# Kernel tuning notes

Measured on AMD Instinct MI355X. Metric: run time of the kernel, lower is better.

## Reference

```python
import jax, jax.numpy as jnp
import numpy as np

N_HEAD = 8
D_Q = 1024
D_K = 1024  # d_k_original
DK = D_K // N_HEAD  # per-head dim = 128
B = 64
L = 2048


def setup_inputs() -> dict:
    key = jax.random.key(0)
    ks = jax.random.split(key, 8)
    std_q = np.sqrt(2.0 / (D_Q + DK)).astype(np.float32)
    std_k = np.sqrt(2.0 / (D_K + DK)).astype(np.float32)
    return {
        "q": jax.random.normal(ks[0], (B, D_Q), jnp.float32),
        "k": jax.random.normal(ks[1], (B, L, D_K), jnp.float32),
        "mask": jnp.zeros((B, L), jnp.bool_),
        # Linear weights stored torch-style: (out_features, in_features)
        "w_qs_w": jax.random.normal(ks[2], (N_HEAD * DK, D_Q), jnp.float32) * std_q,
        "w_qs_b": jnp.zeros((N_HEAD * DK,), jnp.float32),
        "w_ks_w": jax.random.normal(ks[3], (N_HEAD * DK, D_K), jnp.float32) * std_k,
        "w_ks_b": jnp.zeros((N_HEAD * DK,), jnp.float32),
        "w_vs_w": jax.random.normal(ks[4], (N_HEAD * DK, D_K), jnp.float32) * std_k,
        "w_vs_b": jnp.zeros((N_HEAD * DK,), jnp.float32),
    }


def reference(q, k, mask, w_qs_w, w_qs_b, w_ks_w, w_ks_b, w_vs_w, w_vs_b):
    # Dropouts are identity (eval mode).
    b, l, _ = k.shape
    temperature = jnp.sqrt(jnp.asarray(DK, q.dtype))
    # Projections: torch Linear y = x @ W.T + b
    qs = (q @ w_qs_w.T + w_qs_b).reshape(b, N_HEAD, DK)          # (b, n, dk)
    ks = (k @ w_ks_w.T + w_ks_b).reshape(b, l, N_HEAD, DK)       # (b, l, n, dk)
    vs = (k @ w_vs_w.T + w_vs_b).reshape(b, l, N_HEAD, DK)       # (b, l, n, dv)
    # Single-query per head attention scores: (b, n, l)
    attn = jnp.einsum("bnd,blnd->bnl", qs, ks) / temperature
    attn = jnp.where(mask[:, None, :], -jnp.inf, attn)
    attn = jax.nn.softmax(attn, axis=-1)
    # Weighted sum over l: (b, n, dv) -> (b, n*dv)
    output = jnp.einsum("bnl,blnd->bnd", attn, vs).reshape(b, N_HEAD * DK)
    # attn returned head-major like original: (n*b, l)
    attn_out = attn.transpose(1, 0, 2).reshape(N_HEAD * b, l)
    return (output, attn_out)
```

## Files before the change

kernel.cpp:

```cpp
#include <hip/hip_runtime.h>
#include <hip/hip_bf16.h>
#include <math.h>

#define B 64
#define L 2048
#define C 1024
#define NH 8
#define DK 128
#define SCALE 0.08838834764831845f

template<int CTRL, int RMASK = 0xF>
__device__ __forceinline__ float dppmov(float x) {
    return __int_as_float(__builtin_amdgcn_update_dpp(
        0, __float_as_int(x), CTRL, RMASK, 0xF, true));
}
__device__ __forceinline__ float wave_sum_dpp(float s) {
    s += dppmov<0x111>(s);
    s += dppmov<0x112>(s);
    s += dppmov<0x114>(s);
    s += dppmov<0x118>(s);
    s += dppmov<0x142, 0xa>(s);
    s += dppmov<0x143, 0xc>(s);
    return s;
}

__global__ void k_qs(const float* __restrict__ q, const float* __restrict__ wq,
                     const float* __restrict__ bq, float* __restrict__ qs) {
    int t = threadIdx.x, w = t >> 6, lane = t & 63;
    int j = blockIdx.x * 4 + w;
    float4 W[4];
#pragma unroll
    for (int kk = 0; kk < 4; kk++)
        W[kk] = *(const float4*)&wq[(size_t)j * C + kk * 256 + lane * 4];
    float bj = bq[j];
    for (int b = 0; b < B; b++) {
        float s = 0.f;
#pragma unroll
        for (int kk = 0; kk < 4; kk++) {
            float4 qv = *(const float4*)&q[(size_t)b * C + kk * 256 + lane * 4];
            s += W[kk].x * qv.x + W[kk].y * qv.y + W[kk].z * qv.z + W[kk].w * qv.w;
        }
        s = wave_sum_dpp(s);
        if (lane == 63) qs[(size_t)b * C + j] = s + bj;
    }
}

__global__ void k_qtilde(const float* __restrict__ qs, const float* __restrict__ wk,
                         float* __restrict__ qtilde) {
    int n = blockIdx.x >> 2, cc = blockIdx.x & 3, bg = blockIdx.y;
    int t = threadIdx.x;
    int c = cc * 256 + t;
    __shared__ float qss[8][128];
    for (int p = 0; p < 4; p++) {
        int e = p * 256 + t;
        int i = e >> 7, d = e & 127;
        qss[i][d] = qs[(size_t)(bg * 8 + i) * C + n * DK + d];
    }
    __syncthreads();
    float acc[8];
#pragma unroll
    for (int i = 0; i < 8; i++) acc[i] = 0.f;
    for (int d = 0; d < DK; d += 4) {
        float wv0 = wk[(size_t)(n * DK + d + 0) * C + c];
        float wv1 = wk[(size_t)(n * DK + d + 1) * C + c];
        float wv2 = wk[(size_t)(n * DK + d + 2) * C + c];
        float wv3 = wk[(size_t)(n * DK + d + 3) * C + c];
#pragma unroll
        for (int i = 0; i < 8; i++) {
            acc[i] += qss[i][d + 0] * wv0 + qss[i][d + 1] * wv1
                    + qss[i][d + 2] * wv2 + qss[i][d + 3] * wv3;
        }
    }
#pragma unroll
    for (int i = 0; i < 8; i++)
        qtilde[((size_t)(bg * 8 + i) * NH + n) * C + c] = acc[i] * SCALE;
}

__global__ __launch_bounds__(512, 2) void k_fused9(
    const float* __restrict__ kmat, const float* __restrict__ qtilde,
    const unsigned char* __restrict__ mask,
    float* __restrict__ pout,
    float* __restrict__ accpart,
    float* __restrict__ zpart) {
    const int b = blockIdx.x, lp = blockIdx.y;
    const int t = threadIdx.x, w = t >> 6, lane = t & 63;
    const int chunk = w >> 1;
    const int hg = w & 1;
    const int l0 = lp * 512 + chunk * 128;
    const int hl = lane & 3;

    __shared__ float ctxl[NH * C];
    __shared__ float zl[NH];

    float4 qt[4][4];
#pragma unroll
    for (int j = 0; j < 4; j++)
#pragma unroll
        for (int kk = 0; kk < 4; kk++)
            qt[j][kk] = *(const float4*)&qtilde[((size_t)b * NH + hg * 4 + j) * C + kk * 256 + lane * 4];

    float4 acc[4][4];
#pragma unroll
    for (int j = 0; j < 4; j++)
#pragma unroll
        for (int kk = 0; kk < 4; kk++) acc[j][kk] = make_float4(0.f, 0.f, 0.f, 0.f);
    float zacc = 0.f;

    const float* kp = kmat + ((size_t)b * L + l0) * C + lane * 4;
    const unsigned char* mp = mask + (size_t)b * L + l0;

    float4 kv[2][4];
#pragma unroll
    for (int kk = 0; kk < 4; kk++) kv[0][kk] = *(const float4*)(kp + kk * 256);

    for (int rb = 0; rb < 32; rb++) {
        uchar4 mb = *(const uchar4*)&mp[rb * 4];
        float ss[4];
#pragma unroll
        for (int rr = 0; rr < 4; rr++) {
            const int r = rb * 4 + rr;
            const int cur = r & 1;
            if (r < 127) {
                const float* np = kp + (size_t)(r + 1) * C;
#pragma unroll
                for (int kk = 0; kk < 4; kk++)
                    kv[cur ^ 1][kk] = *(const float4*)(np + kk * 256);
            }
            float s0 = 0.f, s1 = 0.f, s2 = 0.f, s3 = 0.f;
#pragma unroll
            for (int kk = 0; kk < 4; kk++) {
                float4 kq = kv[cur][kk];
                s0 += qt[0][kk].x * kq.x + qt[0][kk].y * kq.y + qt[0][kk].z * kq.z + qt[0][kk].w * kq.w;
                s1 += qt[1][kk].x * kq.x + qt[1][kk].y * kq.y + qt[1][kk].z * kq.z + qt[1][kk].w * kq.w;
                s2 += qt[2][kk].x * kq.x + qt[2][kk].y * kq.y + qt[2][kk].z * kq.z + qt[2][kk].w * kq.w;
                s3 += qt[3][kk].x * kq.x + qt[3][kk].y * kq.y + qt[3][kk].z * kq.z + qt[3][kk].w * kq.w;
            }
            float a01 = (lane & 1) ? s1 : s0;
            float g01 = (lane & 1) ? s0 : s1;
            float a23 = (lane & 1) ? s3 : s2;
            float g23 = (lane & 1) ? s2 : s3;
            float u  = a01 + dppmov<0xB1>(g01);
            float v2 = a23 + dppmov<0xB1>(g23);
            float keep = (lane & 2) ? v2 : u;
            float give = (lane & 2) ? u : v2;
            float v = keep + dppmov<0x4E>(give);
            v += dppmov<0x124>(v);
            v += dppmov<0x128>(v);
            v += __int_as_float(__builtin_amdgcn_ds_swizzle(
                     __float_as_int(v), 0x401F));
            v += __shfl_xor(v, 32, 64);
            unsigned char mk = (rr == 0) ? mb.x : (rr == 1) ? mb.y : (rr == 2) ? mb.z : mb.w;
            float p = __expf(mk ? -INFINITY : v);
            zacc += p;
            ss[rr] = p;
            float p1 = dppmov<0xB1>(p);
            float p2 = dppmov<0x4E>(p);
            float p3 = dppmov<0x4E>(p1);
#pragma unroll
            for (int kk = 0; kk < 4; kk++) {
                float4 kq = kv[cur][kk];
                acc[0][kk].x += p  * kq.x; acc[0][kk].y += p  * kq.y; acc[0][kk].z += p  * kq.z; acc[0][kk].w += p  * kq.w;
                acc[1][kk].x += p1 * kq.x; acc[1][kk].y += p1 * kq.y; acc[1][kk].z += p1 * kq.z; acc[1][kk].w += p1 * kq.w;
                acc[2][kk].x += p2 * kq.x; acc[2][kk].y += p2 * kq.y; acc[2][kk].z += p2 * kq.z; acc[2][kk].w += p2 * kq.w;
                acc[3][kk].x += p3 * kq.x; acc[3][kk].y += p3 * kq.y; acc[3][kk].z += p3 * kq.z; acc[3][kk].w += p3 * kq.w;
            }
        }
        if (lane < 4) {
            float4 o = make_float4(ss[0], ss[1], ss[2], ss[3]);
            *(float4*)&pout[((size_t)(hg * 4 + lane) * B + b) * L + l0 + rb * 4] = o;
        }
        __syncthreads();
    }

    for (int ph = 0; ph < 4; ph++) {
        if (chunk == ph) {
#pragma unroll
            for (int j = 0; j < 4; j++) {
                int h = hg * 4 + (hl ^ j);
                float* dst = &ctxl[(size_t)h * C + lane * 4];
                if (ph == 0) {
#pragma unroll
                    for (int kk = 0; kk < 4; kk++)
                        *(float4*)&dst[kk * 256] = acc[j][kk];
                } else {
#pragma unroll
                    for (int kk = 0; kk < 4; kk++) {
                        float4 o = *(const float4*)&dst[kk * 256];
                        float4 a = acc[j][kk];
                        o.x += a.x; o.y += a.y; o.z += a.z; o.w += a.w;
                        *(float4*)&dst[kk * 256] = o;
                    }
                }
            }
            if (lane < 4) {
                if (ph == 0) zl[hg * 4 + lane] = zacc;
                else         zl[hg * 4 + lane] += zacc;
            }
        }
        __syncthreads();
    }
    float* ap = accpart + ((size_t)b * 4 + lp) * (NH * C);
#pragma unroll
    for (int i = 0; i < 4; i++) {
        int idx = t * 16 + i * 4;
        *(float4*)&ap[idx] = *(const float4*)&ctxl[idx];
    }
    if (t < NH) zpart[((size_t)b * 4 + lp) * NH + t] = zl[t];
}

__global__ void k_combine2(const float* __restrict__ accpart, const float* __restrict__ zpart,
                           float* __restrict__ ctx, float* __restrict__ pout) {
    int b = blockIdx.x, cq = blockIdx.y;
    int t = threadIdx.x;
    int c = cq * 256 + t;
    __shared__ float zi[NH];
    if (t < NH) {
        float z = 0.f;
#pragma unroll
        for (int lpp = 0; lpp < 4; lpp++) z += zpart[((size_t)b * 4 + lpp) * NH + t];
        zi[t] = 1.0f / z;
    }
    __syncthreads();
#pragma unroll
    for (int n = 0; n < NH; n++) {
        float s = 0.f;
#pragma unroll
        for (int lpp = 0; lpp < 4; lpp++)
            s += accpart[(((size_t)b * 4 + lpp) * NH + n) * C + c];
        ctx[((size_t)b * NH + n) * C + c] = s * zi[n];
    }
#pragma unroll
    for (int n = 0; n < NH; n++) {
        float zin = zi[n];
        float2* pp = (float2*)&pout[((size_t)n * B + b) * L + cq * 512];
        float2 v = pp[t];
        v.x *= zin; v.y *= zin;
        pp[t] = v;
    }
}

__global__ void k_out(const float* __restrict__ ctx, const float* __restrict__ wv,
                      const float* __restrict__ bv, float* __restrict__ out) {
    int t = threadIdx.x, w = t >> 6, lane = t & 63;
    int j = blockIdx.x * 4 + w;
    int n = j >> 7;
    float4 W[4];
#pragma unroll
    for (int kk = 0; kk < 4; kk++)
        W[kk] = *(const float4*)&wv[(size_t)j * C + kk * 256 + lane * 4];
    float bj = bv[j];
    for (int b = 0; b < B; b++) {
        float s = 0.f;
#pragma unroll
        for (int kk = 0; kk < 4; kk++) {
            float4 cv = *(const float4*)&ctx[((size_t)b * NH + n) * C + kk * 256 + lane * 4];
            s += W[kk].x * cv.x + W[kk].y * cv.y + W[kk].z * cv.z + W[kk].w * cv.w;
        }
        s = wave_sum_dpp(s);
        if (lane == 63) out[(size_t)b * (NH * DK) + j] = s + bj;
    }
}

extern "C" void kernel_launch(void* const* d_in, const int* in_sizes, int n_in,
                              void* d_out, int out_size, void* d_ws, size_t ws_size,
                              hipStream_t stream) {
    const float* q    = (const float*)d_in[0];
    const float* kmat = (const float*)d_in[1];
    const unsigned char* mask = (const unsigned char*)d_in[2];
    const float* wq = (const float*)d_in[3];
    const float* bq = (const float*)d_in[4];
    const float* wk = (const float*)d_in[5];
    const float* wv = (const float*)d_in[7];
    const float* bv = (const float*)d_in[8];

    float* out  = (float*)d_out;
    float* attn = out + B * NH * DK;

    float* ws      = (float*)d_ws;
    float* qs      = ws;
    float* zpart   = ws;
    float* qtilde  = ws + 65536;
    float* ctx     = qtilde;
    float* accpart = ws + 65536 + 524288;

    hipLaunchKernelGGL(k_qs, dim3(256), dim3(256), 0, stream, q, wq, bq, qs);
    hipLaunchKernelGGL(k_qtilde, dim3(32, 8), dim3(256), 0, stream, qs, wk, qtilde);
    hipLaunchKernelGGL(k_fused9, dim3(64, 4), dim3(512), 0, stream,
                       kmat, qtilde, mask, attn, accpart, zpart);
    hipLaunchKernelGGL(k_combine2, dim3(64, 4), dim3(256), 0, stream,
                       accpart, zpart, ctx, attn);
    hipLaunchKernelGGL(k_out, dim3(256), dim3(256), 0, stream, ctx, wv, bv, out);
}
```

Baseline: 228.0 us.

## Deepen K row prefetch to two-row pairs and drop per-block barrier

The main fused kernel now keeps four K rows in registers as two ping-pong pairs, prefetching the next two rows while the current two are processed, instead of a single-row lookahead. It also removes the __syncthreads executed every 4-row block inside the streaming loop, leaving one barrier before the shared-memory reduction. This aims to put more memory loads in flight and stop waves from stalling each other. The extra 32 VGPRs of K buffering may raise register pressure under the 512x2 launch bound and risk spills.

```diff
diff --git a/kernel.cpp b/kernel.cpp
--- a/kernel.cpp
+++ b/kernel.cpp
@@ -76,7 +76,7 @@
         qtilde[((size_t)(bg * 8 + i) * NH + n) * C + c] = acc[i] * SCALE;
 }
 
-__global__ __launch_bounds__(512, 2) void k_fused9(
+__global__ __launch_bounds__(512, 2) void k_fused10(
     const float* __restrict__ kmat, const float* __restrict__ qtilde,
     const unsigned char* __restrict__ mask,
     float* __restrict__ pout,
@@ -109,69 +109,85 @@
     const float* kp = kmat + ((size_t)b * L + l0) * C + lane * 4;
     const unsigned char* mp = mask + (size_t)b * L + l0;
 
-    float4 kv[2][4];
-#pragma unroll
-    for (int kk = 0; kk < 4; kk++) kv[0][kk] = *(const float4*)(kp + kk * 256);
+    auto ROW = [&](const float4 (&kq4)[4], unsigned char mk, float& ssl) {
+        float s0 = 0.f, s1 = 0.f, s2 = 0.f, s3 = 0.f;
+#pragma unroll
+        for (int kk = 0; kk < 4; kk++) {
+            float4 kq = kq4[kk];
+            s0 += qt[0][kk].x * kq.x + qt[0][kk].y * kq.y + qt[0][kk].z * kq.z + qt[0][kk].w * kq.w;
+            s1 += qt[1][kk].x * kq.x + qt[1][kk].y * kq.y + qt[1][kk].z * kq.z + qt[1][kk].w * kq.w;
+            s2 += qt[2][kk].x * kq.x + qt[2][kk].y * kq.y + qt[2][kk].z * kq.z + qt[2][kk].w * kq.w;
+            s3 += qt[3][kk].x * kq.x + qt[3][kk].y * kq.y + qt[3][kk].z * kq.z + qt[3][kk].w * kq.w;
+        }
+        float a01 = (lane & 1) ? s1 : s0;
+        float g01 = (lane & 1) ? s0 : s1;
+        float a23 = (lane & 1) ? s3 : s2;
+        float g23 = (lane & 1) ? s2 : s3;
+        float u  = a01 + dppmov<0xB1>(g01);
+        float v2 = a23 + dppmov<0xB1>(g23);
+        float keep = (lane & 2) ? v2 : u;
+        float give = (lane & 2) ? u : v2;
+        float v = keep + dppmov<0x4E>(give);
+        v += dppmov<0x124>(v);
+        v += dppmov<0x128>(v);
+        v += __int_as_float(__builtin_amdgcn_ds_swizzle(
+                 __float_as_int(v), 0x401F));
+        v += __shfl_xor(v, 32, 64);
+        float p = __expf(mk ? -INFINITY : v);
+        zacc += p;
+        ssl = p;
+        float p1 = dppmov<0xB1>(p);
+        float p2 = dppmov<0x4E>(p);
+        float p3 = dppmov<0x4E>(p1);
+#pragma unroll
+        for (int kk = 0; kk < 4; kk++) {
+            float4 kq = kq4[kk];
+            acc[0][kk].x += p  * kq.x; acc[0][kk].y += p  * kq.y; acc[0][kk].z += p  * kq.z; acc[0][kk].w += p  * kq.w;
+            acc[1][kk].x += p1 * kq.x; acc[1][kk].y += p1 * kq.y; acc[1][kk].z += p1 * kq.z; acc[1][kk].w += p1 * kq.w;
+            acc[2][kk].x += p2 * kq.x; acc[2][kk].y += p2 * kq.y; acc[2][kk].z += p2 * kq.z; acc[2][kk].w += p2 * kq.w;
+            acc[3][kk].x += p3 * kq.x; acc[3][kk].y += p3 * kq.y; acc[3][kk].z += p3 * kq.z; acc[3][kk].w += p3 * kq.w;
+        }
+    };
+
+    float4 kA[2][4], kB[2][4];
+#pragma unroll
+    for (int kk = 0; kk < 4; kk++) {
+        kA[0][kk] = *(const float4*)(kp + 0 * C + kk * 256);
+        kA[1][kk] = *(const float4*)(kp + 1 * C + kk * 256);
+        kB[0][kk] = *(const float4*)(kp + 2 * C + kk * 256);
+        kB[1][kk] = *(const float4*)(kp + 3 * C + kk * 256);
+    }
 
     for (int rb = 0; rb < 32; rb++) {
         uchar4 mb = *(const uchar4*)&mp[rb * 4];
         float ss[4];
-#pragma unroll
-        for (int rr = 0; rr < 4; rr++) {
-            const int r = rb * 4 + rr;
-            const int cur = r & 1;
-            if (r < 127) {
-                const float* np = kp + (size_t)(r + 1) * C;
-#pragma unroll
-                for (int kk = 0; kk < 4; kk++)
-                    kv[cur ^ 1][kk] = *(const float4*)(np + kk * 256);
+        ROW(kA[0], mb.x, ss[0]);
+        ROW(kA[1], mb.y, ss[1]);
+        if (rb < 31) {
+            const float* np = kp + (size_t)(rb * 4 + 4) * C;
+#pragma unroll
+            for (int kk = 0; kk < 4; kk++) {
+                kA[0][kk] = *(const float4*)(np + kk * 256);
+                kA[1][kk] = *(const float4*)(np + C + kk * 256);
             }
-            float s0 = 0.f, s1 = 0.f, s2 = 0.f, s3 = 0.f;
+        }
+        ROW(kB[0], mb.z, ss[2]);
+        ROW(kB[1], mb.w, ss[3]);
+        if (rb < 31) {
+            const float* np = kp + (size_t)(rb * 4 + 6) * C;
 #pragma unroll
             for (int kk = 0; kk < 4; kk++) {
-                float4 kq = kv[cur][kk];
-                s0 += qt[0][kk].x * kq.x + qt[0][kk].y * kq.y + qt[0][kk].z * kq.z + qt[0][kk].w * kq.w;
-                s1 += qt[1][kk].x * kq.x + qt[1][kk].y * kq.y + qt[1][kk].z * kq.z + qt[1][kk].w * kq.w;
-                s2 += qt[2][kk].x * kq.x + qt[2][kk].y * kq.y + qt[2][kk].z * kq.z + qt[2][kk].w * kq.w;
-                s3 += qt[3][kk].x * kq.x + qt[3][kk].y * kq.y + qt[3][kk].z * kq.z + qt[3][kk].w * kq.w;
-            }
-            float a01 = (lane & 1) ? s1 : s0;
-            float g01 = (lane & 1) ? s0 : s1;
-            float a23 = (lane & 1) ? s3 : s2;
-            float g23 = (lane & 1) ? s2 : s3;
-            float u  = a01 + dppmov<0xB1>(g01);
-            float v2 = a23 + dppmov<0xB1>(g23);
-            float keep = (lane & 2) ? v2 : u;
-            float give = (lane & 2) ? u : v2;
-            float v = keep + dppmov<0x4E>(give);
-            v += dppmov<0x124>(v);
-            v += dppmov<0x128>(v);
-            v += __int_as_float(__builtin_amdgcn_ds_swizzle(
-                     __float_as_int(v), 0x401F));
-            v += __shfl_xor(v, 32, 64);
-            unsigned char mk = (rr == 0) ? mb.x : (rr == 1) ? mb.y : (rr == 2) ? mb.z : mb.w;
-            float p = __expf(mk ? -INFINITY : v);
-            zacc += p;
-            ss[rr] = p;
-            float p1 = dppmov<0xB1>(p);
-            float p2 = dppmov<0x4E>(p);
-            float p3 = dppmov<0x4E>(p1);
-#pragma unroll
-            for (int kk = 0; kk < 4; kk++) {
-                float4 kq = kv[cur][kk];
-                acc[0][kk].x += p  * kq.x; acc[0][kk].y += p  * kq.y; acc[0][kk].z += p  * kq.z; acc[0][kk].w += p  * kq.w;
-                acc[1][kk].x += p1 * kq.x; acc[1][kk].y += p1 * kq.y; acc[1][kk].z += p1 * kq.z; acc[1][kk].w += p1 * kq.w;
-                acc[2][kk].x += p2 * kq.x; acc[2][kk].y += p2 * kq.y; acc[2][kk].z += p2 * kq.z; acc[2][kk].w += p2 * kq.w;
-                acc[3][kk].x += p3 * kq.x; acc[3][kk].y += p3 * kq.y; acc[3][kk].z += p3 * kq.z; acc[3][kk].w += p3 * kq.w;
+                kB[0][kk] = *(const float4*)(np + kk * 256);
+                kB[1][kk] = *(const float4*)(np + C + kk * 256);
             }
         }
         if (lane < 4) {
             float4 o = make_float4(ss[0], ss[1], ss[2], ss[3]);
             *(float4*)&pout[((size_t)(hg * 4 + lane) * B + b) * L + l0 + rb * 4] = o;
         }
-        __syncthreads();
-    }
-
+    }
+
+    __syncthreads();
     for (int ph = 0; ph < 4; ph++) {
         if (chunk == ph) {
 #pragma unroll
@@ -285,7 +301,7 @@
 
     hipLaunchKernelGGL(k_qs, dim3(256), dim3(256), 0, stream, q, wq, bq, qs);
     hipLaunchKernelGGL(k_qtilde, dim3(32, 8), dim3(256), 0, stream, qs, wk, qtilde);
-    hipLaunchKernelGGL(k_fused9, dim3(64, 4), dim3(512), 0, stream,
+    hipLaunchKernelGGL(k_fused10, dim3(64, 4), dim3(512), 0, stream,
                        kmat, qtilde, mask, attn, accpart, zpart);
     hipLaunchKernelGGL(k_combine2, dim3(64, 4), dim3(256), 0, stream,
                        accpart, zpart, ctx, attn);
```

New measurement: 416.9 us. 82.9% more time.
